# Performance work log

Hardware: AMD Instinct MI355X
Metric: run time of the kernel (lower is better)

Reference implementation:

```python
import jax, jax.numpy as jnp
import numpy as np

EMBED_DIM = 1024
NUM_HEADS = 16
D_K = EMBED_DIM // NUM_HEADS


def setup_inputs() -> dict:
    key = jax.random.key(0)
    kx, kq, kk, kv, ko = jax.random.split(key, 5)
    scale = 1.0 / np.sqrt(EMBED_DIM)
    return {
        "x": jax.random.normal(kx, (4, 2048, EMBED_DIM), dtype=jnp.float32),
        "w_q": jax.random.normal(kq, (EMBED_DIM, EMBED_DIM), dtype=jnp.float32) * scale,
        "w_k": jax.random.normal(kk, (EMBED_DIM, EMBED_DIM), dtype=jnp.float32) * scale,
        "w_v": jax.random.normal(kv, (EMBED_DIM, EMBED_DIM), dtype=jnp.float32) * scale,
        "w_o": jax.random.normal(ko, (EMBED_DIM, EMBED_DIM), dtype=jnp.float32) * scale,
    }


def reference(x, w_q, w_k, w_v, w_o):
    b, s, _ = x.shape
    # torch nn.Linear: y = x @ W^T
    def proj(w):
        return (x @ w.T).reshape(b, s, NUM_HEADS, D_K).transpose(0, 2, 1, 3)  # [b,h,s,d]
    q, k, v = proj(w_q), proj(w_k), proj(w_v)
    scores = jnp.einsum("bhqd,bhkd->bhqk", q, k) / jnp.sqrt(jnp.float32(D_K))
    attn = jax.nn.softmax(scores, axis=-1)
    out = jnp.einsum("bhqk,bhkd->bhqd", attn, v)
    out = out.transpose(0, 2, 1, 3).reshape(b, s, EMBED_DIM)
    return out @ w_o.T
```

## Files before the change

kernel.cpp:

```cpp
#include <hip/hip_runtime.h>
#include <stdint.h>

#define DEV __device__ __forceinline__

typedef __bf16 bf16x8 __attribute__((ext_vector_type(8)));
typedef float  f32x4  __attribute__((ext_vector_type(4)));
typedef unsigned short us8 __attribute__((ext_vector_type(8)));

DEV unsigned short f2bf(float f) {
  union { float f; uint32_t u; } v; v.f = f;
  uint32_t u = v.u;
  return (unsigned short)((u + 0x7FFFu + ((u >> 16) & 1u)) >> 16);
}

#define GLOAD16(gp, lp) __builtin_amdgcn_global_load_lds( \
    (__attribute__((address_space(1))) void*)(gp),        \
    (__attribute__((address_space(3))) void*)(lp), 16, 0, 0)

__global__ void cvt_f32_bf16(const float* __restrict__ in,
                             unsigned short* __restrict__ out, int n4) {
  int i = blockIdx.x * blockDim.x + threadIdx.x;
  const int stride = gridDim.x * blockDim.x;
  for (; i < n4; i += stride) {
    float4 f = reinterpret_cast<const float4*>(in)[i];
    ushort4 o;
    o.x = f2bf(f.x); o.y = f2bf(f.y); o.z = f2bf(f.z); o.w = f2bf(f.w);
    reinterpret_cast<ushort4*>(out)[i] = o;
  }
}

__global__ void cvt_w4(const float* __restrict__ w0, const float* __restrict__ w1,
                       const float* __restrict__ w2, const float* __restrict__ w3,
                       unsigned short* __restrict__ o0, unsigned short* __restrict__ o1,
                       unsigned short* __restrict__ o2, unsigned short* __restrict__ o3,
                       int n4) {
  const float* in; unsigned short* out;
  switch (blockIdx.y) {
    case 0: in = w0; out = o0; break;
    case 1: in = w1; out = o1; break;
    case 2: in = w2; out = o2; break;
    default: in = w3; out = o3; break;
  }
  int i = blockIdx.x * blockDim.x + threadIdx.x;
  const int stride = gridDim.x * blockDim.x;
  for (; i < n4; i += stride) {
    float4 f = reinterpret_cast<const float4*>(in)[i];
    ushort4 o;
    o.x = f2bf(f.x); o.y = f2bf(f.y); o.z = f2bf(f.z); o.w = f2bf(f.w);
    reinterpret_cast<ushort4*>(out)[i] = o;
  }
}

template<int MODE>
__global__ __launch_bounds__(256, 2) void gemm_bt(
    const unsigned short* __restrict__ A,
    const unsigned short* __restrict__ Bt,
    void* __restrict__ Cout, int M, int N, int K)
{
  __shared__ __align__(16) unsigned short As[128 * 32];
  __shared__ __align__(16) unsigned short Bs[128 * 32];
  const int t    = threadIdx.x;
  const int lane = t & 63;
  const int w    = t >> 6;
  const int wm   = w >> 1, wn = w & 1;
  const int brow = blockIdx.y * 128;
  const int bcol = blockIdx.x * 128;
  const int lr   = lane & 15;
  const int lk   = lane >> 4;
  const int srow = t >> 2;
  const int scol = (t & 3) * 8;

  f32x4 acc[4][4] = {};

  for (int kt = 0; kt < K; kt += 32) {
    __syncthreads();
    GLOAD16(A  + (size_t)(brow + srow)      * K + kt + scol, As + t * 8);
    GLOAD16(A  + (size_t)(brow + 64 + srow) * K + kt + scol, As + 2048 + t * 8);
    GLOAD16(Bt + (size_t)(bcol + srow)      * K + kt + scol, Bs + t * 8);
    GLOAD16(Bt + (size_t)(bcol + 64 + srow) * K + kt + scol, Bs + 2048 + t * 8);
    __syncthreads();

    bf16x8 af[4], bfr[4];
#pragma unroll
    for (int mi = 0; mi < 4; ++mi)
      af[mi] = *reinterpret_cast<const bf16x8*>(As + (wm * 64 + mi * 16 + lr) * 32 + lk * 8);
#pragma unroll
    for (int ni = 0; ni < 4; ++ni)
      bfr[ni] = *reinterpret_cast<const bf16x8*>(Bs + (wn * 64 + ni * 16 + lr) * 32 + lk * 8);
#pragma unroll
    for (int mi = 0; mi < 4; ++mi)
#pragma unroll
      for (int ni = 0; ni < 4; ++ni)
        acc[mi][ni] = __builtin_amdgcn_mfma_f32_16x16x32_bf16(af[mi], bfr[ni], acc[mi][ni], 0, 0, 0);
  }

#pragma unroll
  for (int mi = 0; mi < 4; ++mi) {
    const int row0 = brow + wm * 64 + mi * 16 + lk * 4;
#pragma unroll
    for (int ni = 0; ni < 4; ++ni) {
      const int col = bcol + wn * 64 + ni * 16 + lr;
#pragma unroll
      for (int rr = 0; rr < 4; ++rr) {
        const int row = row0 + rr;
        const float vv = acc[mi][ni][rr];
        if (MODE == 0) {
          ((unsigned short*)Cout)[(size_t)row * N + col] = f2bf(vv);
        } else if (MODE == 2) {
          ((float*)Cout)[(size_t)row * N + col] = vv;
        } else {
          const int bb = row >> 11, ss = row & 2047;
          const int hh = col >> 6,  dd = col & 63;
          ((unsigned short*)Cout)[(size_t)((bb * 16 + hh) * 64 + dd) * 2048 + ss] = f2bf(vv);
        }
      }
    }
  }
}

__global__ __launch_bounds__(256, 3) void attn_fwd(
    const __bf16* __restrict__ Q,
    const __bf16* __restrict__ Kg,
    const __bf16* __restrict__ Vt,
    __bf16* __restrict__ O)
{
  __shared__ __align__(16) __bf16 Kl[64 * 64];
  __shared__ __align__(16) __bf16 Vl[64 * 64];
  __shared__ __align__(16) __bf16 Pl[4][32 * 64];
  const int t    = threadIdx.x;
  const int lane = t & 63;
  const int w    = t >> 6;
  const int lr   = lane & 15;
  const int lk   = lane >> 4;

  const int raw  = blockIdx.x + 16 * blockIdx.y + 256 * blockIdx.z;
  const int xcd  = raw & 7;
  const int slot = raw >> 3;
  const int g    = xcd * 8 + (slot >> 4);
  const int qt   = slot & 15;
  const int b    = g >> 4;
  const int h    = g & 15;
  const int q0   = qt * 128 + w * 32;
  const size_t qrow0 = (size_t)b * 2048 + q0;

  char* Klc = (char*)Kl;
  char* Vlc = (char*)Vl;
  char* Plc = (char*)&Pl[w][0];

  const float qs = 0.125f * 1.44269504f;
  bf16x8 qf[2][2];
#pragma unroll
  for (int m16 = 0; m16 < 2; ++m16)
#pragma unroll
    for (int kk = 0; kk < 2; ++kk) {
      bf16x8 raw8 = *reinterpret_cast<const bf16x8*>(
          Q + (qrow0 + m16 * 16 + lr) * 1024 + h * 64 + kk * 32 + lk * 8);
      bf16x8 tmp;
#pragma unroll
      for (int j = 0; j < 8; ++j) tmp[j] = (__bf16)((float)raw8[j] * qs);
      qf[m16][kk] = tmp;
    }

  f32x4 oacc[2][4] = {};
  f32x4 psum[2] = {};

  const __bf16* Kbase = Kg + (size_t)b * 2048 * 1024 + h * 64;
  const __bf16* Vbase = Vt + (size_t)((b * 16 + h) * 64) * 2048;
  const int sr = t >> 3;
  const int sc = (t & 7) * 8;

  us8 kreg[2], vreg[2];
#pragma unroll
  for (int p = 0; p < 2; ++p) {
    const int row = p * 32 + sr;
    kreg[p] = *reinterpret_cast<const us8*>(Kbase + (size_t)row * 1024 + sc);
    vreg[p] = *reinterpret_cast<const us8*>(Vbase + (size_t)row * 2048 + sc);
  }

  for (int kv0 = 0; kv0 < 2048; kv0 += 64) {
    __syncthreads();
#pragma unroll
    for (int p = 0; p < 2; ++p) {
      const int row = p * 32 + sr;
      const int sw  = ((row * 128 + (t & 7) * 16) ^ ((row & 7) << 4));
      *reinterpret_cast<us8*>(Klc + sw) = kreg[p];
      *reinterpret_cast<us8*>(Vlc + sw) = vreg[p];
    }
    __syncthreads();

    if (kv0 + 64 < 2048) {
      const int nkv = kv0 + 64;
#pragma unroll
      for (int p = 0; p < 2; ++p) {
        const int row = p * 32 + sr;
        kreg[p] = *reinterpret_cast<const us8*>(Kbase + (size_t)(nkv + row) * 1024 + sc);
        vreg[p] = *reinterpret_cast<const us8*>(Vbase + (size_t)row * 2048 + nkv + sc);
      }
    }

    f32x4 sacc[2][4] = {};
#pragma unroll
    for (int ni = 0; ni < 4; ++ni) {
      const int krow = ni * 16 + lr;
      bf16x8 kf0 = *reinterpret_cast<const bf16x8*>(
          Klc + ((krow * 128 + lk * 16) ^ ((krow & 7) << 4)));
      bf16x8 kf1 = *reinterpret_cast<const bf16x8*>(
          Klc + ((krow * 128 + 64 + lk * 16) ^ ((krow & 7) << 4)));
#pragma unroll
      for (int m16 = 0; m16 < 2; ++m16) {
        sacc[m16][ni] = __builtin_amdgcn_mfma_f32_16x16x32_bf16(qf[m16][0], kf0, sacc[m16][ni], 0, 0, 0);
        sacc[m16][ni] = __builtin_amdgcn_mfma_f32_16x16x32_bf16(qf[m16][1], kf1, sacc[m16][ni], 0, 0, 0);
      }
    }

#pragma unroll
    for (int m16 = 0; m16 < 2; ++m16) {
#pragma unroll
      for (int ni = 0; ni < 4; ++ni) {
        f32x4 p;
#pragma unroll
        for (int rr = 0; rr < 4; ++rr) p[rr] = __builtin_amdgcn_exp2f(sacc[m16][ni][rr]);
        psum[m16] += p;
#pragma unroll
        for (int rr = 0; rr < 4; ++rr) {
          const int prow = m16 * 16 + lk * 4 + rr;
          const int pcol = ni * 16 + lr;
          *reinterpret_cast<__bf16*>(
              Plc + ((prow * 128 + pcol * 2) ^ ((prow & 7) << 4))) = (__bf16)p[rr];
        }
      }
    }

    asm volatile("s_waitcnt lgkmcnt(0)" ::: "memory");
    __builtin_amdgcn_sched_barrier(0);

#pragma unroll
    for (int kk = 0; kk < 2; ++kk) {
      bf16x8 pf[2];
#pragma unroll
      for (int m16 = 0; m16 < 2; ++m16) {
        const int prow = m16 * 16 + lr;
        pf[m16] = *reinterpret_cast<const bf16x8*>(
            Plc + ((prow * 128 + kk * 64 + lk * 16) ^ ((prow & 7) << 4)));
      }
#pragma unroll
      for (int d16 = 0; d16 < 4; ++d16) {
        const int vrow = d16 * 16 + lr;
        bf16x8 vf = *reinterpret_cast<const bf16x8*>(
            Vlc + ((vrow * 128 + kk * 64 + lk * 16) ^ ((vrow & 7) << 4)));
        oacc[0][d16] = __builtin_amdgcn_mfma_f32_16x16x32_bf16(pf[0], vf, oacc[0][d16], 0, 0, 0);
        oacc[1][d16] = __builtin_amdgcn_mfma_f32_16x16x32_bf16(pf[1], vf, oacc[1][d16], 0, 0, 0);
      }
    }
  }

#pragma unroll
  for (int m16 = 0; m16 < 2; ++m16) {
#pragma unroll
    for (int rr = 0; rr < 4; ++rr) {
      float s = psum[m16][rr];
      s += __shfl_xor(s, 1);
      s += __shfl_xor(s, 2);
      s += __shfl_xor(s, 4);
      s += __shfl_xor(s, 8);
      const float inv = 1.f / s;
      const int prow = m16 * 16 + lk * 4 + rr;
#pragma unroll
      for (int d16 = 0; d16 < 4; ++d16)
        *reinterpret_cast<__bf16*>(Plc + prow * 128 + (d16 * 16 + lr) * 2) =
            (__bf16)(oacc[m16][d16][rr] * inv);
    }
  }
  asm volatile("s_waitcnt lgkmcnt(0)" ::: "memory");
  __builtin_amdgcn_sched_barrier(0);
  {
    const int er = lane >> 3;
    const int ec = (lane & 7) * 8;
#pragma unroll
    for (int p = 0; p < 4; ++p) {
      const int lrow = p * 8 + er;
      us8 vv = *reinterpret_cast<const us8*>(Plc + lrow * 128 + ec * 2);
      *reinterpret_cast<us8*>(
          (unsigned short*)O + (qrow0 + lrow) * 1024 + h * 64 + ec) = vv;
    }
  }
}

extern "C" void kernel_launch(void* const* d_in, const int* in_sizes, int n_in,
                              void* d_out, int out_size, void* d_ws, size_t ws_size,
                              hipStream_t stream) {
  const float* x  = (const float*)d_in[0];
  const float* wq = (const float*)d_in[1];
  const float* wk = (const float*)d_in[2];
  const float* wv = (const float*)d_in[3];
  const float* wo = (const float*)d_in[4];
  float* out = (float*)d_out;
  uint8_t* ws = (uint8_t*)d_ws;
  const size_t MB = 1024 * 1024;
  unsigned short* xb  = (unsigned short*)(ws + 0);
  unsigned short* wqb = (unsigned short*)(ws + 16 * MB);
  unsigned short* wkb = (unsigned short*)(ws + 18 * MB);
  unsigned short* wvb = (unsigned short*)(ws + 20 * MB);
  unsigned short* wob = (unsigned short*)(ws + 22 * MB);
  unsigned short* Qb  = (unsigned short*)(ws + 24 * MB);
  unsigned short* Kb  = (unsigned short*)(ws + 40 * MB);
  unsigned short* Vtb = (unsigned short*)(ws + 56 * MB);
  unsigned short* Ob  = xb;

  cvt_f32_bf16<<<2048, 256, 0, stream>>>(x, xb, (4 * 2048 * 1024) / 4);
  cvt_w4<<<dim3(256, 4), 256, 0, stream>>>(wq, wk, wv, wo, wqb, wkb, wvb, wob,
                                           (1024 * 1024) / 4);

  dim3 gg(1024 / 128, 8192 / 128);
  gemm_bt<0><<<gg, 256, 0, stream>>>(xb, wqb, Qb,  8192, 1024, 1024);
  gemm_bt<0><<<gg, 256, 0, stream>>>(xb, wkb, Kb,  8192, 1024, 1024);
  gemm_bt<1><<<gg, 256, 0, stream>>>(xb, wvb, Vtb, 8192, 1024, 1024);

  attn_fwd<<<dim3(16, 16, 4), 256, 0, stream>>>(
      (const __bf16*)Qb, (const __bf16*)Kb, (const __bf16*)Vtb, (__bf16*)Ob);

  gemm_bt<2><<<gg, 256, 0, stream>>>(Ob, wob, out, 8192, 1024, 1024);
}
```

Before: 309.0 us.

## Fuse QKV projections into one GEMM and use 32x32 MFMA register-resident attention

The three separate Q/K/V projection GEMM launches are merged into a single gemm_qkv launch over a 24-column-tile grid, which assumes the wq/wk/wv bf16 buffers sit contiguously in the workspace. The attention kernel moves from 16x16x32 to 32x32x16 MFMA and computes S^T = K·Q^T, so the probabilities stay in registers. It packs them with v_cvt_pk_bf16_f32 and swaps lane halves with cross-lane shuffles instead of round-tripping through a per-wave LDS P buffer. This removes the P LDS traffic and shared-memory footprint, and the output staging reuses the K/V LDS tiles. The costs are extra shuffles and higher register pressure from 16-wide accumulators.

Result: faster. 300.1 us (-2.9%).

```diff
diff --git a/kernel.cpp b/kernel.cpp
--- a/kernel.cpp
+++ b/kernel.cpp
@@ -5,12 +5,19 @@
 
 typedef __bf16 bf16x8 __attribute__((ext_vector_type(8)));
 typedef float  f32x4  __attribute__((ext_vector_type(4)));
+typedef float  f32x16 __attribute__((ext_vector_type(16)));
 typedef unsigned short us8 __attribute__((ext_vector_type(8)));
 
 DEV unsigned short f2bf(float f) {
   union { float f; uint32_t u; } v; v.f = f;
   uint32_t u = v.u;
   return (unsigned short)((u + 0x7FFFu + ((u >> 16) & 1u)) >> 16);
+}
+
+DEV uint32_t cvtpk(float lo, float hi) {
+  uint32_t r;
+  asm("v_cvt_pk_bf16_f32 %0, %1, %2" : "=v"(r) : "v"(lo), "v"(hi));
+  return r;
 }
 
 #define GLOAD16(gp, lp) __builtin_amdgcn_global_load_lds( \
@@ -104,14 +111,80 @@
       for (int rr = 0; rr < 4; ++rr) {
         const int row = row0 + rr;
         const float vv = acc[mi][ni][rr];
-        if (MODE == 0) {
+        if (MODE == 2) {
+          ((float*)Cout)[(size_t)row * N + col] = vv;
+        } else {
           ((unsigned short*)Cout)[(size_t)row * N + col] = f2bf(vv);
-        } else if (MODE == 2) {
-          ((float*)Cout)[(size_t)row * N + col] = vv;
+        }
+      }
+    }
+  }
+}
+
+__global__ __launch_bounds__(256, 2) void gemm_qkv(
+    const unsigned short* __restrict__ A,
+    const unsigned short* __restrict__ Bt,
+    unsigned short* __restrict__ Qo,
+    unsigned short* __restrict__ Ko,
+    unsigned short* __restrict__ Vto)
+{
+  __shared__ __align__(16) unsigned short As[128 * 32];
+  __shared__ __align__(16) unsigned short Bs[128 * 32];
+  const int K    = 1024;
+  const int t    = threadIdx.x;
+  const int lane = t & 63;
+  const int w    = t >> 6;
+  const int wm   = w >> 1, wn = w & 1;
+  const int brow = blockIdx.y * 128;
+  const int bcol = blockIdx.x * 128;
+  const int lr   = lane & 15;
+  const int lk   = lane >> 4;
+  const int srow = t >> 2;
+  const int scol = (t & 3) * 8;
+
+  f32x4 acc[4][4] = {};
+
+  for (int kt = 0; kt < K; kt += 32) {
+    __syncthreads();
+    GLOAD16(A  + (size_t)(brow + srow)      * K + kt + scol, As + t * 8);
+    GLOAD16(A  + (size_t)(brow + 64 + srow) * K + kt + scol, As + 2048 + t * 8);
+    GLOAD16(Bt + (size_t)(bcol + srow)      * K + kt + scol, Bs + t * 8);
+    GLOAD16(Bt + (size_t)(bcol + 64 + srow) * K + kt + scol, Bs + 2048 + t * 8);
+    __syncthreads();
+
+    bf16x8 af[4], bfr[4];
+#pragma unroll
+    for (int mi = 0; mi < 4; ++mi)
+      af[mi] = *reinterpret_cast<const bf16x8*>(As + (wm * 64 + mi * 16 + lr) * 32 + lk * 8);
+#pragma unroll
+    for (int ni = 0; ni < 4; ++ni)
+      bfr[ni] = *reinterpret_cast<const bf16x8*>(Bs + (wn * 64 + ni * 16 + lr) * 32 + lk * 8);
+#pragma unroll
+    for (int mi = 0; mi < 4; ++mi)
+#pragma unroll
+      for (int ni = 0; ni < 4; ++ni)
+        acc[mi][ni] = __builtin_amdgcn_mfma_f32_16x16x32_bf16(af[mi], bfr[ni], acc[mi][ni], 0, 0, 0);
+  }
+
+  const int seg = bcol >> 10;
+  const int cb  = bcol & 1023;
+  unsigned short* outp = (seg == 0) ? Qo : Ko;
+#pragma unroll
+  for (int mi = 0; mi < 4; ++mi) {
+    const int row0 = brow + wm * 64 + mi * 16 + lk * 4;
+#pragma unroll
+    for (int ni = 0; ni < 4; ++ni) {
+      const int col = cb + wn * 64 + ni * 16 + lr;
+#pragma unroll
+      for (int rr = 0; rr < 4; ++rr) {
+        const int row = row0 + rr;
+        const unsigned short hv = f2bf(acc[mi][ni][rr]);
+        if (seg < 2) {
+          outp[(size_t)row * 1024 + col] = hv;
         } else {
           const int bb = row >> 11, ss = row & 2047;
           const int hh = col >> 6,  dd = col & 63;
-          ((unsigned short*)Cout)[(size_t)((bb * 16 + hh) * 64 + dd) * 2048 + ss] = f2bf(vv);
+          Vto[(size_t)((bb * 16 + hh) * 64 + dd) * 2048 + ss] = hv;
         }
       }
     }
@@ -126,12 +199,11 @@
 {
   __shared__ __align__(16) __bf16 Kl[64 * 64];
   __shared__ __align__(16) __bf16 Vl[64 * 64];
-  __shared__ __align__(16) __bf16 Pl[4][32 * 64];
   const int t    = threadIdx.x;
   const int lane = t & 63;
   const int w    = t >> 6;
-  const int lr   = lane & 15;
-  const int lk   = lane >> 4;
+  const int l31  = lane & 31;
+  const int hi5  = lane >> 5;
 
   const int raw  = blockIdx.x + 16 * blockIdx.y + 256 * blockIdx.z;
   const int xcd  = raw & 7;
@@ -140,29 +212,25 @@
   const int qt   = slot & 15;
   const int b    = g >> 4;
   const int h    = g & 15;
-  const int q0   = qt * 128 + w * 32;
-  const size_t qrow0 = (size_t)b * 2048 + q0;
+  const int qbase = b * 2048 + qt * 128 + w * 32;
 
   char* Klc = (char*)Kl;
   char* Vlc = (char*)Vl;
-  char* Plc = (char*)&Pl[w][0];
 
   const float qs = 0.125f * 1.44269504f;
-  bf16x8 qf[2][2];
-#pragma unroll
-  for (int m16 = 0; m16 < 2; ++m16)
-#pragma unroll
-    for (int kk = 0; kk < 2; ++kk) {
-      bf16x8 raw8 = *reinterpret_cast<const bf16x8*>(
-          Q + (qrow0 + m16 * 16 + lr) * 1024 + h * 64 + kk * 32 + lk * 8);
-      bf16x8 tmp;
-#pragma unroll
-      for (int j = 0; j < 8; ++j) tmp[j] = (__bf16)((float)raw8[j] * qs);
-      qf[m16][kk] = tmp;
-    }
-
-  f32x4 oacc[2][4] = {};
-  f32x4 psum[2] = {};
+  bf16x8 qf[4];
+#pragma unroll
+  for (int ks = 0; ks < 4; ++ks) {
+    bf16x8 raw8 = *reinterpret_cast<const bf16x8*>(
+        Q + (size_t)(qbase + l31) * 1024 + h * 64 + ks * 16 + hi5 * 8);
+    bf16x8 tmp;
+#pragma unroll
+    for (int j = 0; j < 8; ++j) tmp[j] = (__bf16)((float)raw8[j] * qs);
+    qf[ks] = tmp;
+  }
+
+  f32x16 oacc[2] = {};
+  float psum = 0.f;
 
   const __bf16* Kbase = Kg + (size_t)b * 2048 * 1024 + h * 64;
   const __bf16* Vbase = Vt + (size_t)((b * 16 + h) * 64) * 2048;
@@ -187,7 +255,6 @@
       *reinterpret_cast<us8*>(Vlc + sw) = vreg[p];
     }
     __syncthreads();
-
     if (kv0 + 64 < 2048) {
       const int nkv = kv0 + 64;
 #pragma unroll
@@ -198,78 +265,62 @@
       }
     }
 
-    f32x4 sacc[2][4] = {};
-#pragma unroll
-    for (int ni = 0; ni < 4; ++ni) {
-      const int krow = ni * 16 + lr;
-      bf16x8 kf0 = *reinterpret_cast<const bf16x8*>(
-          Klc + ((krow * 128 + lk * 16) ^ ((krow & 7) << 4)));
-      bf16x8 kf1 = *reinterpret_cast<const bf16x8*>(
-          Klc + ((krow * 128 + 64 + lk * 16) ^ ((krow & 7) << 4)));
-#pragma unroll
-      for (int m16 = 0; m16 < 2; ++m16) {
-        sacc[m16][ni] = __builtin_amdgcn_mfma_f32_16x16x32_bf16(qf[m16][0], kf0, sacc[m16][ni], 0, 0, 0);
-        sacc[m16][ni] = __builtin_amdgcn_mfma_f32_16x16x32_bf16(qf[m16][1], kf1, sacc[m16][ni], 0, 0, 0);
-      }
-    }
-
-#pragma unroll
-    for (int m16 = 0; m16 < 2; ++m16) {
-#pragma unroll
-      for (int ni = 0; ni < 4; ++ni) {
-        f32x4 p;
-#pragma unroll
-        for (int rr = 0; rr < 4; ++rr) p[rr] = __builtin_amdgcn_exp2f(sacc[m16][ni][rr]);
-        psum[m16] += p;
-#pragma unroll
-        for (int rr = 0; rr < 4; ++rr) {
-          const int prow = m16 * 16 + lk * 4 + rr;
-          const int pcol = ni * 16 + lr;
-          *reinterpret_cast<__bf16*>(
-              Plc + ((prow * 128 + pcol * 2) ^ ((prow & 7) << 4))) = (__bf16)p[rr];
-        }
-      }
-    }
-
-    asm volatile("s_waitcnt lgkmcnt(0)" ::: "memory");
-    __builtin_amdgcn_sched_barrier(0);
-
-#pragma unroll
-    for (int kk = 0; kk < 2; ++kk) {
-      bf16x8 pf[2];
-#pragma unroll
-      for (int m16 = 0; m16 < 2; ++m16) {
-        const int prow = m16 * 16 + lr;
-        pf[m16] = *reinterpret_cast<const bf16x8*>(
-            Plc + ((prow * 128 + kk * 64 + lk * 16) ^ ((prow & 7) << 4)));
-      }
-#pragma unroll
-      for (int d16 = 0; d16 < 4; ++d16) {
-        const int vrow = d16 * 16 + lr;
-        bf16x8 vf = *reinterpret_cast<const bf16x8*>(
-            Vlc + ((vrow * 128 + kk * 64 + lk * 16) ^ ((vrow & 7) << 4)));
-        oacc[0][d16] = __builtin_amdgcn_mfma_f32_16x16x32_bf16(pf[0], vf, oacc[0][d16], 0, 0, 0);
-        oacc[1][d16] = __builtin_amdgcn_mfma_f32_16x16x32_bf16(pf[1], vf, oacc[1][d16], 0, 0, 0);
-      }
-    }
-  }
-
-#pragma unroll
-  for (int m16 = 0; m16 < 2; ++m16) {
-#pragma unroll
-    for (int rr = 0; rr < 4; ++rr) {
-      float s = psum[m16][rr];
-      s += __shfl_xor(s, 1);
-      s += __shfl_xor(s, 2);
-      s += __shfl_xor(s, 4);
-      s += __shfl_xor(s, 8);
-      const float inv = 1.f / s;
-      const int prow = m16 * 16 + lk * 4 + rr;
-#pragma unroll
-      for (int d16 = 0; d16 < 4; ++d16)
-        *reinterpret_cast<__bf16*>(Plc + prow * 128 + (d16 * 16 + lr) * 2) =
-            (__bf16)(oacc[m16][d16][rr] * inv);
-    }
+#pragma unroll
+    for (int st = 0; st < 2; ++st) {
+      const int kvrow = st * 32 + l31;
+      const int kswz  = (kvrow & 7) << 4;
+      f32x16 sacc = {};
+#pragma unroll
+      for (int ks = 0; ks < 4; ++ks) {
+        bf16x8 kf = *reinterpret_cast<const bf16x8*>(
+            Klc + ((kvrow * 128 + ks * 32 + hi5 * 16) ^ kswz));
+        sacc = __builtin_amdgcn_mfma_f32_32x32x16_bf16(kf, qf[ks], sacc, 0, 0, 0);
+      }
+      float p[16];
+#pragma unroll
+      for (int r = 0; r < 16; ++r) {
+        p[r] = __builtin_amdgcn_exp2f(sacc[r]);
+        psum += p[r];
+      }
+      uint32_t c[8], pc[8];
+#pragma unroll
+      for (int k = 0; k < 8; ++k) c[k] = cvtpk(p[2 * k], p[2 * k + 1]);
+#pragma unroll
+      for (int k = 0; k < 8; ++k) pc[k] = (uint32_t)__shfl_xor((int)c[k], 32);
+      union { uint32_t u[4]; bf16x8 v; } pa0, pa1;
+      pa0.u[0] = hi5 ? pc[2] : c[0];
+      pa0.u[1] = hi5 ? pc[3] : c[1];
+      pa0.u[2] = hi5 ? c[2]  : pc[0];
+      pa0.u[3] = hi5 ? c[3]  : pc[1];
+      pa1.u[0] = hi5 ? pc[6] : c[4];
+      pa1.u[1] = hi5 ? pc[7] : c[5];
+      pa1.u[2] = hi5 ? c[6]  : pc[4];
+      pa1.u[3] = hi5 ? c[7]  : pc[5];
+#pragma unroll
+      for (int dt = 0; dt < 2; ++dt) {
+        const int drow = dt * 32 + l31;
+        const int vswz = (drow & 7) << 4;
+        bf16x8 vf0 = *reinterpret_cast<const bf16x8*>(
+            Vlc + ((drow * 128 + st * 64 + hi5 * 16) ^ vswz));
+        bf16x8 vf1 = *reinterpret_cast<const bf16x8*>(
+            Vlc + ((drow * 128 + st * 64 + 32 + hi5 * 16) ^ vswz));
+        oacc[dt] = __builtin_amdgcn_mfma_f32_32x32x16_bf16(pa0.v, vf0, oacc[dt], 0, 0, 0);
+        oacc[dt] = __builtin_amdgcn_mfma_f32_32x32x16_bf16(pa1.v, vf1, oacc[dt], 0, 0, 0);
+      }
+    }
+  }
+
+  psum += __shfl_xor(psum, 32);
+
+  __syncthreads();
+  __bf16* Ob_l = ((w & 2) ? Vl : Kl) + (w & 1) * 2048;
+#pragma unroll
+  for (int r = 0; r < 16; ++r) {
+    const int q = (r & 3) + 8 * (r >> 2) + 4 * hi5;
+    const float s = __shfl(psum, hi5 * 32 + q);
+    const float inv = 1.f / s;
+    Ob_l[q * 64 + l31]      = (__bf16)(oacc[0][r] * inv);
+    Ob_l[q * 64 + 32 + l31] = (__bf16)(oacc[1][r] * inv);
   }
   asm volatile("s_waitcnt lgkmcnt(0)" ::: "memory");
   __builtin_amdgcn_sched_barrier(0);
@@ -279,9 +330,9 @@
 #pragma unroll
     for (int p = 0; p < 4; ++p) {
       const int lrow = p * 8 + er;
-      us8 vv = *reinterpret_cast<const us8*>(Plc + lrow * 128 + ec * 2);
+      us8 vv = *reinterpret_cast<const us8*>(Ob_l + lrow * 64 + ec);
       *reinterpret_cast<us8*>(
-          (unsigned short*)O + (qrow0 + lrow) * 1024 + h * 64 + ec) = vv;
+          (unsigned short*)O + (size_t)(qbase + lrow) * 1024 + h * 64 + ec) = vv;
     }
   }
 }
@@ -311,13 +362,10 @@
   cvt_w4<<<dim3(256, 4), 256, 0, stream>>>(wq, wk, wv, wo, wqb, wkb, wvb, wob,
                                            (1024 * 1024) / 4);
 
-  dim3 gg(1024 / 128, 8192 / 128);
-  gemm_bt<0><<<gg, 256, 0, stream>>>(xb, wqb, Qb,  8192, 1024, 1024);
-  gemm_bt<0><<<gg, 256, 0, stream>>>(xb, wkb, Kb,  8192, 1024, 1024);
-  gemm_bt<1><<<gg, 256, 0, stream>>>(xb, wvb, Vtb, 8192, 1024, 1024);
+  gemm_qkv<<<dim3(24, 64), 256, 0, stream>>>(xb, wqb, Qb, Kb, Vtb);
 
   attn_fwd<<<dim3(16, 16, 4), 256, 0, stream>>>(
       (const __bf16*)Qb, (const __bf16*)Kb, (const __bf16*)Vtb, (__bf16*)Ob);
 
-  gemm_bt<2><<<gg, 256, 0, stream>>>(Ob, wob, out, 8192, 1024, 1024);
-}
+  gemm_bt<2><<<dim3(8, 64), 256, 0, stream>>>(Ob, wob, out, 8192, 1024, 1024);
+}
```
